# Kernel optimization log

Measured on AMD Instinct MI355X. Metric: run time of the kernel, lower is better.

## Reference

```python
import jax, jax.numpy as jnp
import numpy as np

N = 100000          # nodes
E = 1600000         # edges (avg degree 16)
BAG = 10            # feature ids per node
VOCAB = 50000
D_EMB, D_HID, D_OUT = 128, 64, 32


def setup_inputs() -> dict:
    key = jax.random.key(0)
    ks = jax.random.split(key, 10)
    s = lambda d: 1.0 / np.sqrt(d)
    return {
        "feature_indices": jax.random.randint(ks[0], (N * BAG,), 0, VOCAB),
        "feature_offsets": jnp.arange(N, dtype=jnp.int64) * BAG,
        "edge_index": jax.random.randint(ks[1], (2, E), 0, N),
        "emb_table": jax.random.normal(ks[2], (VOCAB, D_EMB), jnp.float32) * 0.02,
        "W1": jax.random.normal(ks[3], (D_EMB, D_HID), jnp.float32) * s(D_EMB),
        "b1": jnp.zeros((D_HID,), jnp.float32),
        "W_mu": jax.random.normal(ks[4], (D_HID, D_OUT), jnp.float32) * s(D_HID),
        "b_mu": jnp.zeros((D_OUT,), jnp.float32),
        "W_ls": jax.random.normal(ks[5], (D_HID, D_OUT), jnp.float32) * s(D_HID),
        "b_ls": jnp.zeros((D_OUT,), jnp.float32),
        "noise": jax.random.normal(ks[6], (N, D_OUT), jnp.float32),
    }


def _embedding_bag_mean(table, indices, offsets, n_bags):
    # torch.nn.EmbeddingBag(mode='mean') with offsets: bag b spans
    # indices[offsets[b] : offsets[b+1]].
    total = indices.shape[0]
    seg = jnp.searchsorted(offsets, jnp.arange(total), side="right") - 1  # [total]
    emb = table[indices]                                                    # [total, D]
    sums = jax.ops.segment_sum(emb, seg, num_segments=n_bags)               # [N, D]
    counts = jnp.diff(jnp.concatenate([offsets, jnp.array([total], offsets.dtype)]))
    return sums / jnp.maximum(counts, 1)[:, None].astype(sums.dtype)


def _gcn_conv(x, W, b, src, dst, norm, n_nodes):
    # GCNConv: linear -> gather -> normalize -> scatter-add -> bias
    h = x @ W                                   # [N, out]
    msg = h[src] * norm[:, None]                # [E+N, out]
    return jax.ops.segment_sum(msg, dst, num_segments=n_nodes) + b


def reference(feature_indices, feature_offsets, edge_index, emb_table,
              W1, b1, W_mu, b_mu, W_ls, b_ls, noise):
    n = noise.shape[0]
    x = _embedding_bag_mean(emb_table, feature_indices, feature_offsets, n)

    # symmetric GCN normalization with self loops (PyG gcn_norm defaults)
    loop = jnp.arange(n)
    src = jnp.concatenate([edge_index[0], loop])
    dst = jnp.concatenate([edge_index[1], loop])
    deg = jax.ops.segment_sum(jnp.ones_like(src, jnp.float32), dst, num_segments=n)
    dinv = jax.lax.rsqrt(jnp.maximum(deg, 1.0))
    norm = dinv[src] * dinv[dst]                # [E+N]

    h = jax.nn.relu(_gcn_conv(x, W1, b1, src, dst, norm, n))
    mu = _gcn_conv(h, W_mu, b_mu, src, dst, norm, n)
    logstd = _gcn_conv(h, W_ls, b_ls, src, dst, norm, n)
    z = mu + noise * jnp.exp(logstd)            # reparameterize

    # decode: edge-wise dot product + sigmoid on the positive edges
    logits = jnp.sum(z[edge_index[0]] * z[edge_index[1]], axis=1)  # [E]
    return jax.nn.sigmoid(logits)
```

## Files before the change

kernel.cpp:

```cpp
#include <hip/hip_runtime.h>
#include <hip/hip_fp16.h>
#include <math.h>

#define DEMB 128
#define DHID 64
#define DOUT 32
#define BAG  10
#define CAP  64
#define BKB  7
#define BKN  128
#define EBLK 8192
#define MAXBKT 1024
#define GROWS 16

typedef unsigned int   u32;
typedef unsigned short u16;

__device__ __forceinline__ u16 f2bf(float f) {
    union { float f; u32 i; } c; c.f = f;
    u32 r = c.i + 0x7FFFu + ((c.i >> 16) & 1u);
    return (u16)(r >> 16);
}
__device__ __forceinline__ void bf2x(u32 v, float& lo, float& hi) {
    union { u32 i; float f; } a, b;
    a.i = v << 16; b.i = v & 0xFFFF0000u;
    lo = a.f; hi = b.f;
}
__device__ __forceinline__ u32 pack2(float f0, float f1) {
    return (u32)f2bf(f0) | ((u32)f2bf(f1) << 16);
}
__device__ __forceinline__ float2 h2f2(u32 v) {
    __half2 h; *reinterpret_cast<u32*>(&h) = v;
    return __half22float2(h);
}
__device__ __forceinline__ u32 f2h2(float a, float b) {
    __half2 h = __floats2half2_rn(a, b);
    return *reinterpret_cast<u32*>(&h);
}
__device__ __forceinline__ u32 hadd2u(u32 a, u32 b) {
    __half2 ha, hb;
    *reinterpret_cast<u32*>(&ha) = a;
    *reinterpret_cast<u32*>(&hb) = b;
    __half2 r = __hadd2(ha, hb);
    return *reinterpret_cast<u32*>(&r);
}
__device__ __forceinline__ u32 hmul2u(u32 a, __half2 s) {
    __half2 ha; *reinterpret_cast<u32*>(&ha) = a;
    __half2 r = __hmul2(ha, s);
    return *reinterpret_cast<u32*>(&r);
}
__device__ __forceinline__ uint4 hadd2u4(uint4 a, uint4 b) {
    a.x = hadd2u(a.x, b.x); a.y = hadd2u(a.y, b.y);
    a.z = hadd2u(a.z, b.z); a.w = hadd2u(a.w, b.w);
    return a;
}

__global__ __launch_bounds__(256) void histA_gemm(const int* __restrict__ dst, int E,
                                                  int* __restrict__ counts, int nblk, int nbkt,
                                                  const float* __restrict__ T,
                                                  const float* __restrict__ W1,
                                                  u16* __restrict__ TW, int V) {
    __shared__ u32 shbuf[DEMB * DHID / 2];
    if ((int)blockIdx.x < nblk) {
        int* hist = (int*)shbuf;
        for (int i = threadIdx.x; i < nbkt; i += 256) hist[i] = 0;
        __syncthreads();
        int base = blockIdx.x * EBLK;
#pragma unroll 4
        for (int k = 0; k < EBLK / 256; ++k) {
            int i = base + k * 256 + threadIdx.x;
            if (i < E) atomicAdd(&hist[dst[i] >> BKB], 1);
        }
        __syncthreads();
        for (int i = threadIdx.x; i < nbkt; i += 256)
            counts[(size_t)i * nblk + blockIdx.x] = hist[i];
        return;
    }
    for (int i = threadIdx.x; i < DEMB * DHID / 2; i += 256) {
        float2 w = reinterpret_cast<const float2*>(W1)[i];
        shbuf[i] = pack2(w.x, w.y);
    }
    __syncthreads();
    int gb = blockIdx.x - nblk;
    int row = gb * GROWS + (threadIdx.x >> 4);
    int cp4 = threadIdx.x & 15;
    if (row >= V) return;
    const float4* t4 = reinterpret_cast<const float4*>(T + (size_t)row * DEMB);
    float a0 = 0.f, a1 = 0.f, a2 = 0.f, a3 = 0.f;
#pragma unroll 4
    for (int k4 = 0; k4 < DEMB / 4; ++k4) {
        float4 t = t4[k4];
        const uint2* wb = reinterpret_cast<const uint2*>(&shbuf[(k4 * 4) * 32 + cp4 * 2]);
        float f0, f1, f2, f3;
        uint2 w;
        w = wb[0];  bf2x(w.x, f0, f1); bf2x(w.y, f2, f3);
        a0 = fmaf(t.x, f0, a0); a1 = fmaf(t.x, f1, a1); a2 = fmaf(t.x, f2, a2); a3 = fmaf(t.x, f3, a3);
        w = wb[16]; bf2x(w.x, f0, f1); bf2x(w.y, f2, f3);
        a0 = fmaf(t.y, f0, a0); a1 = fmaf(t.y, f1, a1); a2 = fmaf(t.y, f2, a2); a3 = fmaf(t.y, f3, a3);
        w = wb[32]; bf2x(w.x, f0, f1); bf2x(w.y, f2, f3);
        a0 = fmaf(t.z, f0, a0); a1 = fmaf(t.z, f1, a1); a2 = fmaf(t.z, f2, a2); a3 = fmaf(t.z, f3, a3);
        w = wb[48]; bf2x(w.x, f0, f1); bf2x(w.y, f2, f3);
        a0 = fmaf(t.w, f0, a0); a1 = fmaf(t.w, f1, a1); a2 = fmaf(t.w, f2, a2); a3 = fmaf(t.w, f3, a3);
    }
    uint2 o;
    o.x = f2h2(a0, a1);
    o.y = f2h2(a2, a3);
    *reinterpret_cast<uint2*>(TW + (size_t)row * DHID + cp4 * 4) = o;
}

__global__ __launch_bounds__(256) void passB1(int* __restrict__ counts, int nblk,
                                              int* __restrict__ btot) {
    __shared__ int sh[256];
    int b = blockIdx.x, t = threadIdx.x;
    int* p = counts + (size_t)b * nblk;
    int v = (t < nblk) ? p[t] : 0;
    sh[t] = v;
    __syncthreads();
    for (int off = 1; off < 256; off <<= 1) {
        int u = (t >= off) ? sh[t - off] : 0;
        __syncthreads();
        sh[t] += u;
        __syncthreads();
    }
    if (t < nblk) p[t] = sh[t] - v;
    if (t == 255) btot[b] = sh[255];
}

__global__ __launch_bounds__(1024) void passB2(const int* __restrict__ btot, int nbkt,
                                               int* __restrict__ rowptr) {
    __shared__ int tot[1024];
    int t = threadIdx.x;
    int v = (t < nbkt) ? btot[t] : 0;
    tot[t] = v;
    __syncthreads();
    for (int off = 1; off < 1024; off <<= 1) {
        int u = (t >= off) ? tot[t - off] : 0;
        __syncthreads();
        tot[t] += u;
        __syncthreads();
    }
    if (t < nbkt) rowptr[t] = tot[t] - v;
    if (t == nbkt - 1) rowptr[nbkt] = tot[t];
}

__global__ __launch_bounds__(256) void passC_bag(const int* __restrict__ src,
                                                 const int* __restrict__ dst, int E,
                                                 const int* __restrict__ counts, int nblk,
                                                 const int* __restrict__ rowptr, int nbkt,
                                                 u32* __restrict__ bbuf,
                                                 const int* __restrict__ idx,
                                                 const u16* __restrict__ TW,
                                                 u16* __restrict__ h0, int n) {
    if ((int)blockIdx.x < nblk) {
        __shared__ int hist[MAXBKT];
        __shared__ int off0[MAXBKT];
        int blk = blockIdx.x;
        for (int i = threadIdx.x; i < nbkt; i += 256) {
            hist[i] = 0;
            off0[i] = rowptr[i] + counts[(size_t)i * nblk + blk];
        }
        __syncthreads();
        int base = blk * EBLK;
#pragma unroll 4
        for (int k = 0; k < EBLK / 256; ++k) {
            int i = base + k * 256 + threadIdx.x;
            if (i < E) {
                int d = dst[i], s = src[i];
                int bk = d >> BKB;
                int l = atomicAdd(&hist[bk], 1);
                bbuf[off0[bk] + l] = (u32)s | ((u32)(d & (BKN - 1)) << 17);
            }
        }
        return;
    }
    int t = (blockIdx.x - nblk) * 256 + threadIdx.x;
    int node = t >> 3, d8 = t & 7;
    if (node >= n) return;
    const int* bi = idx + (size_t)node * BAG;
    uint4 acc = make_uint4(0u, 0u, 0u, 0u);
#pragma unroll
    for (int j = 0; j < BAG; ++j) {
        uint4 v = *reinterpret_cast<const uint4*>(TW + (size_t)bi[j] * DHID + d8 * 8);
        acc = hadd2u4(acc, v);
    }
    const __half2 s2 = __floats2half2_rn(0.1f, 0.1f);
    acc.x = hmul2u(acc.x, s2);
    acc.y = hmul2u(acc.y, s2);
    acc.z = hmul2u(acc.z, s2);
    acc.w = hmul2u(acc.w, s2);
    *reinterpret_cast<uint4*>(h0 + (size_t)node * DHID + d8 * 8) = acc;
}

__global__ __launch_bounds__(256) void adj_build(const u32* __restrict__ bbuf,
                                                 const int* __restrict__ rowptr,
                                                 int* __restrict__ adj,
                                                 int* __restrict__ degc,
                                                 u16* __restrict__ h0, int n) {
    __shared__ int cnt[BKN];
    __shared__ __align__(16) int adjS[BKN * CAP];
    const int b = blockIdx.x, tid = threadIdx.x;
    if (tid < BKN) cnt[tid] = 0;
    __syncthreads();
    int s0 = rowptr[b], s1 = rowptr[b + 1];
    for (int i = s0 + tid; i < s1; i += 256) {
        u32 v = bbuf[i];
        int dl = v >> 17;
        int r = atomicAdd(&cnt[dl], 1);
        if (r < CAP) adjS[dl * CAP + r] = (int)(v & 0x1FFFF);
    }
    __syncthreads();
    const int base = b * BKN;
    int nn = n - base; if (nn > BKN) nn = BKN;
    int tot4 = nn * (CAP / 4);
    int4* gout = reinterpret_cast<int4*>(adj + (size_t)base * CAP);
    const int4* lin = reinterpret_cast<const int4*>(adjS);
    for (int i = tid; i < tot4; i += 256) {
        int row = i >> 4, s = i & 15;
        if (s * 4 < cnt[row]) gout[i] = lin[i];
    }
    int row = tid >> 1, half = tid & 1;
    int node = base + row;
    if (node < n) {
        int dc = cnt[row];
        if (half == 0) degc[node] = dc;
        float di = rsqrtf((float)(dc + 1));
        __half2 di2 = __floats2half2_rn(di, di);
        uint4* hp = reinterpret_cast<uint4*>(h0 + (size_t)node * DHID + half * 32);
#pragma unroll
        for (int q = 0; q < 4; ++q) {
            uint4 v = hp[q];
            v.x = hmul2u(v.x, di2);
            v.y = hmul2u(v.y, di2);
            v.z = hmul2u(v.z, di2);
            v.w = hmul2u(v.w, di2);
            hp[q] = v;
        }
    }
}

__global__ __launch_bounds__(256) void conv1mm(const u16* __restrict__ h0,
                                               const int* __restrict__ degc,
                                               const int* __restrict__ adj,
                                               const float* __restrict__ b1,
                                               const float* __restrict__ Wmu,
                                               const float* __restrict__ Wls,
                                               u16* __restrict__ hcat, int n) {
    __shared__ u16 Wp[DHID * DHID];
    for (int i = threadIdx.x; i < DHID * DHID; i += 256) {
        int k = i >> 6, p = i & 63;
        int j = p >> 3, c = p & 7;
        float w = (c < 4) ? Wmu[k * DOUT + j * 4 + c] : Wls[k * DOUT + j * 4 + (c - 4)];
        Wp[i] = f2bf(w);
    }
    __syncthreads();
    int t = blockIdx.x * 256 + threadIdx.x;
    int node = t >> 3, d8 = t & 7;
    if (node >= n) return;
    int dc = degc[node];
    int deg = dc < CAP ? dc : CAP;
    const int* ap = adj + (size_t)node * CAP;
    const int4* ap4 = reinterpret_cast<const int4*>(ap);
    uint4 acc = *reinterpret_cast<const uint4*>(h0 + (size_t)node * DHID + d8 * 8);
    int k = 0;
    for (; k + 8 <= deg; k += 8) {
        int4 s0 = ap4[k >> 2], s1 = ap4[(k >> 2) + 1];
        uint4 v0 = *reinterpret_cast<const uint4*>(h0 + (size_t)s0.x * DHID + d8 * 8);
        uint4 v1 = *reinterpret_cast<const uint4*>(h0 + (size_t)s0.y * DHID + d8 * 8);
        uint4 v2 = *reinterpret_cast<const uint4*>(h0 + (size_t)s0.z * DHID + d8 * 8);
        uint4 v3 = *reinterpret_cast<const uint4*>(h0 + (size_t)s0.w * DHID + d8 * 8);
        uint4 v4 = *reinterpret_cast<const uint4*>(h0 + (size_t)s1.x * DHID + d8 * 8);
        uint4 v5 = *reinterpret_cast<const uint4*>(h0 + (size_t)s1.y * DHID + d8 * 8);
        uint4 v6 = *reinterpret_cast<const uint4*>(h0 + (size_t)s1.z * DHID + d8 * 8);
        uint4 v7 = *reinterpret_cast<const uint4*>(h0 + (size_t)s1.w * DHID + d8 * 8);
        v0 = hadd2u4(v0, v1); v2 = hadd2u4(v2, v3);
        v4 = hadd2u4(v4, v5); v6 = hadd2u4(v6, v7);
        v0 = hadd2u4(v0, v2); v4 = hadd2u4(v4, v6);
        acc = hadd2u4(acc, hadd2u4(v0, v4));
    }
    for (; k + 4 <= deg; k += 4) {
        int4 s0 = ap4[k >> 2];
        uint4 v0 = *reinterpret_cast<const uint4*>(h0 + (size_t)s0.x * DHID + d8 * 8);
        uint4 v1 = *reinterpret_cast<const uint4*>(h0 + (size_t)s0.y * DHID + d8 * 8);
        uint4 v2 = *reinterpret_cast<const uint4*>(h0 + (size_t)s0.z * DHID + d8 * 8);
        uint4 v3 = *reinterpret_cast<const uint4*>(h0 + (size_t)s0.w * DHID + d8 * 8);
        v0 = hadd2u4(v0, v1); v2 = hadd2u4(v2, v3);
        acc = hadd2u4(acc, hadd2u4(v0, v2));
    }
    for (; k < deg; ++k) {
        uint4 v = *reinterpret_cast<const uint4*>(h0 + (size_t)ap[k] * DHID + d8 * 8);
        acc = hadd2u4(acc, v);
    }
    float di = rsqrtf((float)(dc + 1));
    float4 b0 = *reinterpret_cast<const float4*>(b1 + d8 * 8);
    float4 b4 = *reinterpret_cast<const float4*>(b1 + d8 * 8 + 4);
    float2 q0 = h2f2(acc.x), q1 = h2f2(acc.y), q2 = h2f2(acc.z), q3 = h2f2(acc.w);
    float pr[8];
    pr[0] = fmaxf(fmaf(di, q0.x, b0.x), 0.f);
    pr[1] = fmaxf(fmaf(di, q0.y, b0.y), 0.f);
    pr[2] = fmaxf(fmaf(di, q1.x, b0.z), 0.f);
    pr[3] = fmaxf(fmaf(di, q1.y, b0.w), 0.f);
    pr[4] = fmaxf(fmaf(di, q2.x, b4.x), 0.f);
    pr[5] = fmaxf(fmaf(di, q2.y, b4.y), 0.f);
    pr[6] = fmaxf(fmaf(di, q3.x, b4.z), 0.f);
    pr[7] = fmaxf(fmaf(di, q3.y, b4.w), 0.f);
    float oa[8] = {0.f, 0.f, 0.f, 0.f, 0.f, 0.f, 0.f, 0.f};
#pragma unroll
    for (int kk = 0; kk < DHID; ++kk) {
        float hv = __shfl(pr[kk & 7], kk >> 3, 8);
        uint4 wv = *reinterpret_cast<const uint4*>(&Wp[kk * DHID + d8 * 8]);
        float f0, f1;
        bf2x(wv.x, f0, f1); oa[0] = fmaf(hv, f0, oa[0]); oa[1] = fmaf(hv, f1, oa[1]);
        bf2x(wv.y, f0, f1); oa[2] = fmaf(hv, f0, oa[2]); oa[3] = fmaf(hv, f1, oa[3]);
        bf2x(wv.z, f0, f1); oa[4] = fmaf(hv, f0, oa[4]); oa[5] = fmaf(hv, f1, oa[5]);
        bf2x(wv.w, f0, f1); oa[6] = fmaf(hv, f0, oa[6]); oa[7] = fmaf(hv, f1, oa[7]);
    }
    uint4 o;
    o.x = f2h2(oa[0] * di, oa[1] * di);
    o.y = f2h2(oa[2] * di, oa[3] * di);
    o.z = f2h2(oa[4] * di, oa[5] * di);
    o.w = f2h2(oa[6] * di, oa[7] * di);
    *reinterpret_cast<uint4*>(hcat + (size_t)node * DHID + d8 * 8) = o;
}

__global__ void gather_conv2(const u16* __restrict__ hcat, const int* __restrict__ degc,
                             const int* __restrict__ adj,
                             const float* __restrict__ bmu, const float* __restrict__ bls,
                             const float* __restrict__ noise, __half* __restrict__ z, int n) {
    int t = blockIdx.x * blockDim.x + threadIdx.x;
    int node = t >> 3, j = t & 7;
    if (node >= n) return;
    int dc = degc[node];
    int deg = dc < CAP ? dc : CAP;
    const int* ap = adj + (size_t)node * CAP;
    const int4* ap4 = reinterpret_cast<const int4*>(ap);
    uint4 acc = *reinterpret_cast<const uint4*>(hcat + (size_t)node * DHID + j * 8);
    int k = 0;
    for (; k + 8 <= deg; k += 8) {
        int4 s0 = ap4[k >> 2], s1 = ap4[(k >> 2) + 1];
        uint4 v0 = *reinterpret_cast<const uint4*>(hcat + (size_t)s0.x * DHID + j * 8);
        uint4 v1 = *reinterpret_cast<const uint4*>(hcat + (size_t)s0.y * DHID + j * 8);
        uint4 v2 = *reinterpret_cast<const uint4*>(hcat + (size_t)s0.z * DHID + j * 8);
        uint4 v3 = *reinterpret_cast<const uint4*>(hcat + (size_t)s0.w * DHID + j * 8);
        uint4 v4 = *reinterpret_cast<const uint4*>(hcat + (size_t)s1.x * DHID + j * 8);
        uint4 v5 = *reinterpret_cast<const uint4*>(hcat + (size_t)s1.y * DHID + j * 8);
        uint4 v6 = *reinterpret_cast<const uint4*>(hcat + (size_t)s1.z * DHID + j * 8);
        uint4 v7 = *reinterpret_cast<const uint4*>(hcat + (size_t)s1.w * DHID + j * 8);
        v0 = hadd2u4(v0, v1); v2 = hadd2u4(v2, v3);
        v4 = hadd2u4(v4, v5); v6 = hadd2u4(v6, v7);
        v0 = hadd2u4(v0, v2); v4 = hadd2u4(v4, v6);
        acc = hadd2u4(acc, hadd2u4(v0, v4));
    }
    for (; k + 4 <= deg; k += 4) {
        int4 s0 = ap4[k >> 2];
        uint4 v0 = *reinterpret_cast<const uint4*>(hcat + (size_t)s0.x * DHID + j * 8);
        uint4 v1 = *reinterpret_cast<const uint4*>(hcat + (size_t)s0.y * DHID + j * 8);
        uint4 v2 = *reinterpret_cast<const uint4*>(hcat + (size_t)s0.z * DHID + j * 8);
        uint4 v3 = *reinterpret_cast<const uint4*>(hcat + (size_t)s0.w * DHID + j * 8);
        v0 = hadd2u4(v0, v1); v2 = hadd2u4(v2, v3);
        acc = hadd2u4(acc, hadd2u4(v0, v2));
    }
    for (; k < deg; ++k) {
        uint4 v = *reinterpret_cast<const uint4*>(hcat + (size_t)ap[k] * DHID + j * 8);
        acc = hadd2u4(acc, v);
    }
    float di = rsqrtf((float)(dc + 1));
    float2 m01 = h2f2(acc.x), m23 = h2f2(acc.y);
    float2 l01 = h2f2(acc.z), l23 = h2f2(acc.w);
    float4 bm = *reinterpret_cast<const float4*>(bmu + j * 4);
    float4 bl = *reinterpret_cast<const float4*>(bls + j * 4);
    float4 nz = *reinterpret_cast<const float4*>(noise + (size_t)node * DOUT + j * 4);
    float z0 = fmaf(di, m01.x, bm.x) + nz.x * expf(fmaf(di, l01.x, bl.x));
    float z1 = fmaf(di, m01.y, bm.y) + nz.y * expf(fmaf(di, l01.y, bl.y));
    float z2 = fmaf(di, m23.x, bm.z) + nz.z * expf(fmaf(di, l23.x, bl.z));
    float z3 = fmaf(di, m23.y, bm.w) + nz.w * expf(fmaf(di, l23.y, bl.w));
    uint2 o;
    o.x = f2h2(z0, z1);
    o.y = f2h2(z2, z3);
    *reinterpret_cast<uint2*>(z + (size_t)node * DOUT + j * 4) = o;
}

__global__ void edge_dot(const __half* __restrict__ z, const int* __restrict__ src,
                         const int* __restrict__ dst, float* __restrict__ out, int E) {
    int t = blockIdx.x * blockDim.x + threadIdx.x;
    int e = t >> 2, q = t & 3;
    if (e >= E) return;
    uint4 a = *reinterpret_cast<const uint4*>(z + (size_t)src[e] * DOUT + q * 8);
    uint4 b = *reinterpret_cast<const uint4*>(z + (size_t)dst[e] * DOUT + q * 8);
    float s = 0.f;
    float2 x, y;
    x = h2f2(a.x); y = h2f2(b.x); s += x.x * y.x + x.y * y.y;
    x = h2f2(a.y); y = h2f2(b.y); s += x.x * y.x + x.y * y.y;
    x = h2f2(a.z); y = h2f2(b.z); s += x.x * y.x + x.y * y.y;
    x = h2f2(a.w); y = h2f2(b.w); s += x.x * y.x + x.y * y.y;
    s += __shfl_xor(s, 1);
    s += __shfl_xor(s, 2);
    if (q == 0) out[e] = 1.0f / (1.0f + expf(-s));
}

extern "C" void kernel_launch(void* const* d_in, const int* in_sizes, int n_in,
                              void* d_out, int out_size, void* d_ws, size_t ws_size,
                              hipStream_t stream) {
    const int*   feat_idx = (const int*)d_in[0];
    const int*   edges    = (const int*)d_in[2];
    const float* table    = (const float*)d_in[3];
    const float* W1       = (const float*)d_in[4];
    const float* b1       = (const float*)d_in[5];
    const float* Wmu      = (const float*)d_in[6];
    const float* bmu      = (const float*)d_in[7];
    const float* Wls      = (const float*)d_in[8];
    const float* bls      = (const float*)d_in[9];
    const float* noise    = (const float*)d_in[10];

    const int N = in_sizes[10] / DOUT;
    const int E = in_sizes[2] / 2;
    const int V = in_sizes[3] / DEMB;

    const int* src = edges;
    const int* dst = edges + E;

    const int NBKT = (N + BKN - 1) / BKN;
    const int NBLK = (E + EBLK - 1) / EBLK;

    char* ws = (char*)d_ws;
    size_t off = 0;
    auto alloc = [&](size_t bytes) { char* p = ws + off; off += (bytes + 255) & ~size_t(255); return p; };
    u16*    tableW = (u16*)   alloc((size_t)V * DHID * 2);
    u16*    h0     = (u16*)   alloc((size_t)N * DHID * 2);
    u16*    hcat   = (u16*)   alloc((size_t)N * DHID * 2);
    __half* zbuf   = (__half*)alloc((size_t)N * DOUT * 2);
    int*    adj    = (int*)   alloc((size_t)N * CAP * 4);
    u32*    bbuf   = (u32*)   alloc((size_t)E * 4);
    int*    counts = (int*)   alloc((size_t)NBKT * NBLK * 4);
    int*    rowptr = (int*)   alloc((size_t)(NBKT + 1) * 4);
    int*    btot   = (int*)   alloc((size_t)NBKT * 4);
    int*    degc   = (int*)   alloc((size_t)N * 4);
    (void)ws_size;

    const int B = 256;
    const int nbg = (V + GROWS - 1) / GROWS;
    const int nbe = ((long long)N * 8 + B - 1) / B;

    histA_gemm<<<NBLK + nbg, B, 0, stream>>>(dst, E, counts, NBLK, NBKT,
                                             table, W1, tableW, V);
    passB1<<<NBKT, B, 0, stream>>>(counts, NBLK, btot);
    passB2<<<1, 1024, 0, stream>>>(btot, NBKT, rowptr);
    passC_bag<<<NBLK + nbe, B, 0, stream>>>(src, dst, E, counts, NBLK, rowptr, NBKT,
                                            bbuf, feat_idx, tableW, h0, N);
    adj_build<<<NBKT, B, 0, stream>>>(bbuf, rowptr, adj, degc, h0, N);

    conv1mm<<<(N + 31) / 32, B, 0, stream>>>(h0, degc, adj, b1, Wmu, Wls, hcat, N);

    {
        long long t = (long long)N * 8;
        gather_conv2<<<(unsigned)((t + B - 1) / B), B, 0, stream>>>(hcat, degc, adj,
                                                                    bmu, bls, noise, zbuf, N);
    }
    {
        long long t = (long long)E * 4;
        edge_dot<<<(unsigned)((t + B - 1) / B), B, 0, stream>>>(zbuf, src, dst, (float*)d_out, E);
    }
}
```

Before: 191.5 us.

## Partition adjacency lists into source-id ranges to localize neighbor gathers

The adjacency build now splits each node's neighbor list into three sub-lists by source-node id range (thresholds N/3, 2N/3), each capped at 32 entries, and stores per-range counts plus the total degree as an int4. The gather kernels for both convolutions walk the ranges in order through a shared helper, so neighbor gathers cluster in address space to improve cache hit rates on h0/hcat. This enlarges the adjacency array and its LDS staging buffer (96 slots per node), adds more loop overhead per node, and changes the truncation semantics from a single 64 cap to per-range 32 caps.

```diff
diff --git a/kernel.cpp b/kernel.cpp
--- a/kernel.cpp
+++ b/kernel.cpp
@@ -6,7 +6,9 @@
 #define DHID 64
 #define DOUT 32
 #define BAG  10
-#define CAP  64
+#define NR   3
+#define CAPR 32
+#define ROWI (NR * CAPR)
 #define BKB  7
 #define BKN  128
 #define EBLK 8192
@@ -194,35 +196,43 @@
 __global__ __launch_bounds__(256) void adj_build(const u32* __restrict__ bbuf,
                                                  const int* __restrict__ rowptr,
                                                  int* __restrict__ adj,
-                                                 int* __restrict__ degc,
-                                                 u16* __restrict__ h0, int n) {
-    __shared__ int cnt[BKN];
-    __shared__ __align__(16) int adjS[BKN * CAP];
+                                                 int* __restrict__ degr,
+                                                 u16* __restrict__ h0, int n,
+                                                 int t1, int t2) {
+    __shared__ int cnt[NR][BKN];
+    __shared__ __align__(16) int adjS[BKN * ROWI];
     const int b = blockIdx.x, tid = threadIdx.x;
-    if (tid < BKN) cnt[tid] = 0;
+    for (int i = tid; i < NR * BKN; i += 256) ((int*)cnt)[i] = 0;
     __syncthreads();
     int s0 = rowptr[b], s1 = rowptr[b + 1];
     for (int i = s0 + tid; i < s1; i += 256) {
         u32 v = bbuf[i];
+        int s = (int)(v & 0x1FFFF);
         int dl = v >> 17;
-        int r = atomicAdd(&cnt[dl], 1);
-        if (r < CAP) adjS[dl * CAP + r] = (int)(v & 0x1FFFF);
+        int r = (s >= t1) + (s >= t2);
+        int slot = atomicAdd(&cnt[r][dl], 1);
+        if (slot < CAPR) adjS[dl * ROWI + r * CAPR + slot] = s;
     }
     __syncthreads();
     const int base = b * BKN;
     int nn = n - base; if (nn > BKN) nn = BKN;
-    int tot4 = nn * (CAP / 4);
-    int4* gout = reinterpret_cast<int4*>(adj + (size_t)base * CAP);
+    int tot4 = nn * (ROWI / 4);
+    int4* gout = reinterpret_cast<int4*>(adj + (size_t)base * ROWI);
     const int4* lin = reinterpret_cast<const int4*>(adjS);
     for (int i = tid; i < tot4; i += 256) {
-        int row = i >> 4, s = i & 15;
-        if (s * 4 < cnt[row]) gout[i] = lin[i];
+        int row = i / (ROWI / 4), q = i % (ROWI / 4);
+        int r = q >> 3, s = q & 7;
+        if (s * 4 < cnt[r][row]) gout[i] = lin[i];
     }
     int row = tid >> 1, half = tid & 1;
     int node = base + row;
     if (node < n) {
-        int dc = cnt[row];
-        if (half == 0) degc[node] = dc;
+        int c0 = cnt[0][row]; if (c0 > CAPR) c0 = CAPR;
+        int c1 = cnt[1][row]; if (c1 > CAPR) c1 = CAPR;
+        int c2 = cnt[2][row]; if (c2 > CAPR) c2 = CAPR;
+        int dc = cnt[0][row] + cnt[1][row] + cnt[2][row];
+        if (half == 0)
+            *reinterpret_cast<int4*>(degr + (size_t)node * 4) = make_int4(c0, c1, c2, dc);
         float di = rsqrtf((float)(dc + 1));
         __half2 di2 = __floats2half2_rn(di, di);
         uint4* hp = reinterpret_cast<uint4*>(h0 + (size_t)node * DHID + half * 32);
@@ -238,8 +248,49 @@
     }
 }
 
+__device__ __forceinline__ uint4 gather_ranges(const u16* __restrict__ tab,
+                                               const int* __restrict__ ap,
+                                               int4 d3, int lane_off, uint4 acc) {
+#pragma unroll
+    for (int r = 0; r < NR; ++r) {
+        int dr = (r == 0) ? d3.x : (r == 1) ? d3.y : d3.z;
+        const int* seg = ap + r * CAPR;
+        const int4* seg4 = reinterpret_cast<const int4*>(seg);
+        int k = 0;
+        for (; k + 8 <= dr; k += 8) {
+            int4 s0 = seg4[k >> 2], s1 = seg4[(k >> 2) + 1];
+            uint4 v0 = *reinterpret_cast<const uint4*>(tab + (size_t)s0.x * DHID + lane_off);
+            uint4 v1 = *reinterpret_cast<const uint4*>(tab + (size_t)s0.y * DHID + lane_off);
+            uint4 v2 = *reinterpret_cast<const uint4*>(tab + (size_t)s0.z * DHID + lane_off);
+            uint4 v3 = *reinterpret_cast<const uint4*>(tab + (size_t)s0.w * DHID + lane_off);
+            uint4 v4 = *reinterpret_cast<const uint4*>(tab + (size_t)s1.x * DHID + lane_off);
+            uint4 v5 = *reinterpret_cast<const uint4*>(tab + (size_t)s1.y * DHID + lane_off);
+            uint4 v6 = *reinterpret_cast<const uint4*>(tab + (size_t)s1.z * DHID + lane_off);
+            uint4 v7 = *reinterpret_cast<const uint4*>(tab + (size_t)s1.w * DHID + lane_off);
+            v0 = hadd2u4(v0, v1); v2 = hadd2u4(v2, v3);
+            v4 = hadd2u4(v4, v5); v6 = hadd2u4(v6, v7);
+            v0 = hadd2u4(v0, v2); v4 = hadd2u4(v4, v6);
+            acc = hadd2u4(acc, hadd2u4(v0, v4));
+        }
+        for (; k + 4 <= dr; k += 4) {
+            int4 s0 = seg4[k >> 2];
+            uint4 v0 = *reinterpret_cast<const uint4*>(tab + (size_t)s0.x * DHID + lane_off);
+            uint4 v1 = *reinterpret_cast<const uint4*>(tab + (size_t)s0.y * DHID + lane_off);
+            uint4 v2 = *reinterpret_cast<const uint4*>(tab + (size_t)s0.z * DHID + lane_off);
+            uint4 v3 = *reinterpret_cast<const uint4*>(tab + (size_t)s0.w * DHID + lane_off);
+            v0 = hadd2u4(v0, v1); v2 = hadd2u4(v2, v3);
+            acc = hadd2u4(acc, hadd2u4(v0, v2));
+        }
+        for (; k < dr; ++k) {
+            uint4 v = *reinterpret_cast<const uint4*>(tab + (size_t)seg[k] * DHID + lane_off);
+            acc = hadd2u4(acc, v);
+        }
+    }
+    return acc;
+}
+
 __global__ __launch_bounds__(256) void conv1mm(const u16* __restrict__ h0,
-                                               const int* __restrict__ degc,
+                                               const int* __restrict__ degr,
                                                const int* __restrict__ adj,
                                                const float* __restrict__ b1,
                                                const float* __restrict__ Wmu,
@@ -256,40 +307,11 @@
     int t = blockIdx.x * 256 + threadIdx.x;
     int node = t >> 3, d8 = t & 7;
     if (node >= n) return;
-    int dc = degc[node];
-    int deg = dc < CAP ? dc : CAP;
-    const int* ap = adj + (size_t)node * CAP;
-    const int4* ap4 = reinterpret_cast<const int4*>(ap);
+    int4 d3 = *reinterpret_cast<const int4*>(degr + (size_t)node * 4);
+    int dc = d3.w;
+    const int* ap = adj + (size_t)node * ROWI;
     uint4 acc = *reinterpret_cast<const uint4*>(h0 + (size_t)node * DHID + d8 * 8);
-    int k = 0;
-    for (; k + 8 <= deg; k += 8) {
-        int4 s0 = ap4[k >> 2], s1 = ap4[(k >> 2) + 1];
-        uint4 v0 = *reinterpret_cast<const uint4*>(h0 + (size_t)s0.x * DHID + d8 * 8);
-        uint4 v1 = *reinterpret_cast<const uint4*>(h0 + (size_t)s0.y * DHID + d8 * 8);
-        uint4 v2 = *reinterpret_cast<const uint4*>(h0 + (size_t)s0.z * DHID + d8 * 8);
-        uint4 v3 = *reinterpret_cast<const uint4*>(h0 + (size_t)s0.w * DHID + d8 * 8);
-        uint4 v4 = *reinterpret_cast<const uint4*>(h0 + (size_t)s1.x * DHID + d8 * 8);
-        uint4 v5 = *reinterpret_cast<const uint4*>(h0 + (size_t)s1.y * DHID + d8 * 8);
-        uint4 v6 = *reinterpret_cast<const uint4*>(h0 + (size_t)s1.z * DHID + d8 * 8);
-        uint4 v7 = *reinterpret_cast<const uint4*>(h0 + (size_t)s1.w * DHID + d8 * 8);
-        v0 = hadd2u4(v0, v1); v2 = hadd2u4(v2, v3);
-        v4 = hadd2u4(v4, v5); v6 = hadd2u4(v6, v7);
-        v0 = hadd2u4(v0, v2); v4 = hadd2u4(v4, v6);
-        acc = hadd2u4(acc, hadd2u4(v0, v4));
-    }
-    for (; k + 4 <= deg; k += 4) {
-        int4 s0 = ap4[k >> 2];
-        uint4 v0 = *reinterpret_cast<const uint4*>(h0 + (size_t)s0.x * DHID + d8 * 8);
-        uint4 v1 = *reinterpret_cast<const uint4*>(h0 + (size_t)s0.y * DHID + d8 * 8);
-        uint4 v2 = *reinterpret_cast<const uint4*>(h0 + (size_t)s0.z * DHID + d8 * 8);
-        uint4 v3 = *reinterpret_cast<const uint4*>(h0 + (size_t)s0.w * DHID + d8 * 8);
-        v0 = hadd2u4(v0, v1); v2 = hadd2u4(v2, v3);
-        acc = hadd2u4(acc, hadd2u4(v0, v2));
-    }
-    for (; k < deg; ++k) {
-        uint4 v = *reinterpret_cast<const uint4*>(h0 + (size_t)ap[k] * DHID + d8 * 8);
-        acc = hadd2u4(acc, v);
-    }
+    acc = gather_ranges(h0, ap, d3, d8 * 8, acc);
     float di = rsqrtf((float)(dc + 1));
     float4 b0 = *reinterpret_cast<const float4*>(b1 + d8 * 8);
     float4 b4 = *reinterpret_cast<const float4*>(b1 + d8 * 8 + 4);
@@ -322,47 +344,18 @@
     *reinterpret_cast<uint4*>(hcat + (size_t)node * DHID + d8 * 8) = o;
 }
 
-__global__ void gather_conv2(const u16* __restrict__ hcat, const int* __restrict__ degc,
+__global__ void gather_conv2(const u16* __restrict__ hcat, const int* __restrict__ degr,
                              const int* __restrict__ adj,
                              const float* __restrict__ bmu, const float* __restrict__ bls,
                              const float* __restrict__ noise, __half* __restrict__ z, int n) {
     int t = blockIdx.x * blockDim.x + threadIdx.x;
     int node = t >> 3, j = t & 7;
     if (node >= n) return;
-    int dc = degc[node];
-    int deg = dc < CAP ? dc : CAP;
-    const int* ap = adj + (size_t)node * CAP;
-    const int4* ap4 = reinterpret_cast<const int4*>(ap);
+    int4 d3 = *reinterpret_cast<const int4*>(degr + (size_t)node * 4);
+    int dc = d3.w;
+    const int* ap = adj + (size_t)node * ROWI;
     uint4 acc = *reinterpret_cast<const uint4*>(hcat + (size_t)node * DHID + j * 8);
-    int k = 0;
-    for (; k + 8 <= deg; k += 8) {
-        int4 s0 = ap4[k >> 2], s1 = ap4[(k >> 2) + 1];
-        uint4 v0 = *reinterpret_cast<const uint4*>(hcat + (size_t)s0.x * DHID + j * 8);
-        uint4 v1 = *reinterpret_cast<const uint4*>(hcat + (size_t)s0.y * DHID + j * 8);
-        uint4 v2 = *reinterpret_cast<const uint4*>(hcat + (size_t)s0.z * DHID + j * 8);
-        uint4 v3 = *reinterpret_cast<const uint4*>(hcat + (size_t)s0.w * DHID + j * 8);
-        uint4 v4 = *reinterpret_cast<const uint4*>(hcat + (size_t)s1.x * DHID + j * 8);
-        uint4 v5 = *reinterpret_cast<const uint4*>(hcat + (size_t)s1.y * DHID + j * 8);
-        uint4 v6 = *reinterpret_cast<const uint4*>(hcat + (size_t)s1.z * DHID + j * 8);
-        uint4 v7 = *reinterpret_cast<const uint4*>(hcat + (size_t)s1.w * DHID + j * 8);
-        v0 = hadd2u4(v0, v1); v2 = hadd2u4(v2, v3);
-        v4 = hadd2u4(v4, v5); v6 = hadd2u4(v6, v7);
-        v0 = hadd2u4(v0, v2); v4 = hadd2u4(v4, v6);
-        acc = hadd2u4(acc, hadd2u4(v0, v4));
-    }
-    for (; k + 4 <= deg; k += 4) {
-        int4 s0 = ap4[k >> 2];
-        uint4 v0 = *reinterpret_cast<const uint4*>(hcat + (size_t)s0.x * DHID + j * 8);
-        uint4 v1 = *reinterpret_cast<const uint4*>(hcat + (size_t)s0.y * DHID + j * 8);
-        uint4 v2 = *reinterpret_cast<const uint4*>(hcat + (size_t)s0.z * DHID + j * 8);
-        uint4 v3 = *reinterpret_cast<const uint4*>(hcat + (size_t)s0.w * DHID + j * 8);
-        v0 = hadd2u4(v0, v1); v2 = hadd2u4(v2, v3);
-        acc = hadd2u4(acc, hadd2u4(v0, v2));
-    }
-    for (; k < deg; ++k) {
-        uint4 v = *reinterpret_cast<const uint4*>(hcat + (size_t)ap[k] * DHID + j * 8);
-        acc = hadd2u4(acc, v);
-    }
+    acc = gather_ranges(hcat, ap, d3, j * 8, acc);
     float di = rsqrtf((float)(dc + 1));
     float2 m01 = h2f2(acc.x), m23 = h2f2(acc.y);
     float2 l01 = h2f2(acc.z), l23 = h2f2(acc.w);
@@ -420,6 +413,8 @@
 
     const int NBKT = (N + BKN - 1) / BKN;
     const int NBLK = (E + EBLK - 1) / EBLK;
+    const int T1 = (N + NR - 1) / NR;
+    const int T2 = 2 * T1;
 
     char* ws = (char*)d_ws;
     size_t off = 0;
@@ -428,12 +423,12 @@
     u16*    h0     = (u16*)   alloc((size_t)N * DHID * 2);
     u16*    hcat   = (u16*)   alloc((size_t)N * DHID * 2);
     __half* zbuf   = (__half*)alloc((size_t)N * DOUT * 2);
-    int*    adj    = (int*)   alloc((size_t)N * CAP * 4);
+    int*    adj    = (int*)   alloc((size_t)N * ROWI * 4);
     u32*    bbuf   = (u32*)   alloc((size_t)E * 4);
     int*    counts = (int*)   alloc((size_t)NBKT * NBLK * 4);
     int*    rowptr = (int*)   alloc((size_t)(NBKT + 1) * 4);
     int*    btot   = (int*)   alloc((size_t)NBKT * 4);
-    int*    degc   = (int*)   alloc((size_t)N * 4);
+    int*    degr   = (int*)   alloc((size_t)N * 4 * 4);
     (void)ws_size;
 
     const int B = 256;
@@ -446,13 +441,13 @@
     passB2<<<1, 1024, 0, stream>>>(btot, NBKT, rowptr);
     passC_bag<<<NBLK + nbe, B, 0, stream>>>(src, dst, E, counts, NBLK, rowptr, NBKT,
                                             bbuf, feat_idx, tableW, h0, N);
-    adj_build<<<NBKT, B, 0, stream>>>(bbuf, rowptr, adj, degc, h0, N);
-
-    conv1mm<<<(N + 31) / 32, B, 0, stream>>>(h0, degc, adj, b1, Wmu, Wls, hcat, N);
+    adj_build<<<NBKT, B, 0, stream>>>(bbuf, rowptr, adj, degr, h0, N, T1, T2);
+
+    conv1mm<<<(N + 31) / 32, B, 0, stream>>>(h0, degr, adj, b1, Wmu, Wls, hcat, N);
 
     {
         long long t = (long long)N * 8;
-        gather_conv2<<<(unsigned)((t + B - 1) / B), B, 0, stream>>>(hcat, degc, adj,
+        gather_conv2<<<(unsigned)((t + B - 1) / B), B, 0, stream>>>(hcat, degr, adj,
                                                                     bmu, bls, noise, zbuf, N);
     }
     {
```

After: 213.0 us. 11.2% more time.
